# Kernel tuning notes

Hardware: AMD Instinct MI355X
Metric: run time of the kernel (lower is better)

Reference implementation:

```python
import jax, jax.numpy as jnp
import numpy as np

B, L, C, H = 2, 2048, 2048, 16
COND = 2048
HID = 4 * C
LN_EPS = 1e-6


def _ln(x):
    m = jnp.mean(x, axis=-1, keepdims=True)
    v = jnp.mean((x - m) ** 2, axis=-1, keepdims=True)
    return (x - m) / jnp.sqrt(v + LN_EPS)


def _gelu_tanh(u):
    c = np.sqrt(2.0 / np.pi).astype(np.float32)
    return 0.5 * u * (1.0 + jnp.tanh(c * (u + 0.044715 * u ** 3)))


def setup_inputs() -> dict:
    key = jax.random.key(0)
    ks = jax.random.split(key, 8)
    s = 0.02
    return {
        "x": jax.random.normal(ks[0], (B, L, C), jnp.float32),
        "cond_BD": jax.random.normal(ks[1], (B, COND), jnp.float32),
        "attn_bias": jnp.zeros((1, 1, L, L), jnp.float32),
        "Wqkv": (jax.random.normal(ks[2], (3 * C, C), jnp.float32) * s),
        "q_bias": jnp.zeros((C,), jnp.float32),
        "v_bias": jnp.zeros((C,), jnp.float32),
        "scale_mul_log": jnp.full((1, H, 1, 1), np.log(4.0), jnp.float32),
        "Wproj": (jax.random.normal(ks[3], (C, C), jnp.float32) * s),
        "bproj": jnp.zeros((C,), jnp.float32),
        "Wada": (jax.random.normal(ks[4], (6 * C, COND), jnp.float32) * s),
        "bada": jnp.zeros((6 * C,), jnp.float32),
        "Wfc1": (jax.random.normal(ks[5], (HID, C), jnp.float32) * s),
        "bfc1": jnp.zeros((HID,), jnp.float32),
        "Wfc2": (jax.random.normal(ks[6], (C, HID), jnp.float32) * s),
        "bfc2": jnp.zeros((C,), jnp.float32),
    }


def reference(x, cond_BD, attn_bias, Wqkv, q_bias, v_bias, scale_mul_log,
              Wproj, bproj, Wada, bada, Wfc1, bfc1, Wfc2, bfc2):
    Bs, Lx, Cx = x.shape
    D = Cx // H
    # AdaLN modulation: SiLU -> Linear(cond_dim, 6C) -> view(B,1,6,C).unbind(2)
    ada = (jax.nn.silu(cond_BD) @ Wada.T + bada).reshape(Bs, 1, 6, Cx)
    gamma1, gamma2, scale1, scale2, shift1, shift2 = [ada[:, :, i, :] for i in range(6)]

    def attn(xin):
        qkv_bias = jnp.concatenate([q_bias, jnp.zeros_like(q_bias), v_bias])
        qkv = (xin @ Wqkv.T + qkv_bias).reshape(Bs, Lx, 3, H, D)
        qkv = jnp.transpose(qkv, (2, 0, 3, 1, 4))  # [3, B, H, L, D]
        q, k, v = qkv[0], qkv[1], qkv[2]
        # cos-attn: L2-normalize q,k; q scaled by exp(clamped log-scale); softmax scale = 1
        sm = jnp.exp(jnp.minimum(scale_mul_log, jnp.log(jnp.float32(100.0))))
        qn = q / jnp.maximum(jnp.linalg.norm(q, axis=-1, keepdims=True), 1e-12) * sm
        kn = k / jnp.maximum(jnp.linalg.norm(k, axis=-1, keepdims=True), 1e-12)
        scores = jnp.einsum('bhqd,bhkd->bhqk', qn, kn) + attn_bias
        p = jax.nn.softmax(scores, axis=-1)
        o = jnp.einsum('bhqk,bhkd->bhqd', p, v)
        o = jnp.transpose(o, (0, 2, 1, 3)).reshape(Bs, Lx, Cx)
        return o @ Wproj.T + bproj

    x = x + attn(_ln(x) * (scale1 + 1.0) + shift1) * gamma1
    h = _gelu_tanh((_ln(x) * (scale2 + 1.0) + shift2) @ Wfc1.T + bfc1)
    x = x + (h @ Wfc2.T + bfc2) * gamma2
    return x
```

## Files before the change

### kernel.cpp

```cpp
#include <hip/hip_runtime.h>

typedef unsigned short u16;
typedef float f32x4 __attribute__((ext_vector_type(4)));
typedef short short8 __attribute__((ext_vector_type(8)));

#define C_ 2048
#define L_ 2048
#define H_ 16
#define D_ 128
#define SIXC 12288

__device__ __forceinline__ u16 f2bf(float f) {
  union { float f; unsigned u; } v; v.f = f;
  unsigned r = v.u + 0x7FFFu + ((v.u >> 16) & 1u);
  return (u16)(r >> 16);
}
__device__ __forceinline__ float bf2f(u16 b) {
  union { unsigned u; float f; } v; v.u = ((unsigned)b) << 16; return v.f;
}

#define GLOAD_LDS16(g, l)                                            \
  __builtin_amdgcn_global_load_lds(                                  \
      (__attribute__((address_space(1))) void*)(g),                  \
      (__attribute__((address_space(3))) void*)(l), 16, 0, 0)

__global__ __launch_bounds__(256) void conv_bf16(
    const float* __restrict__ src, u16* __restrict__ dst, int n) {
  int i = (blockIdx.x * 256 + threadIdx.x) * 4;
  if (i >= n) return;
  float4 v = *(const float4*)&src[i];
  ushort4 o;
  o.x = f2bf(v.x); o.y = f2bf(v.y); o.z = f2bf(v.z); o.w = f2bf(v.w);
  *(ushort4*)&dst[i] = o;
}

__global__ __launch_bounds__(256) void prep_kernel(
    const float* __restrict__ cond, const float* __restrict__ qb,
    const float* __restrict__ vb, const float* __restrict__ sml,
    float* __restrict__ silu_cond, float* __restrict__ qkvbias,
    float* __restrict__ sm) {
  int i = blockIdx.x * 256 + threadIdx.x;
  if (i < 4096) { float c = cond[i]; silu_cond[i] = c / (1.f + __expf(-c)); }
  if (i < 6144) {
    float bv = (i < 2048) ? qb[i] : ((i < 4096) ? 0.f : vb[i - 4096]);
    qkvbias[i] = bv;
  }
  if (i < 16) sm[i] = __expf(fminf(sml[i], 4.6051701859880914f));
}

__global__ __launch_bounds__(256) void ada_gemm(
    const float* __restrict__ sc, const float* __restrict__ Wada,
    const float* __restrict__ bada, float* __restrict__ ada) {
  int gw = (blockIdx.x * 256 + threadIdx.x) >> 6;
  int lane = threadIdx.x & 63;
  int b = gw / SIXC, row = gw % SIXC;
  const float* s0 = sc + b * 2048;
  const float* w0 = Wada + (size_t)row * 2048;
  float s = 0.f;
  for (int k = lane; k < 2048; k += 64) s = fmaf(s0[k], w0[k], s);
  #pragma unroll
  for (int off = 32; off; off >>= 1) s += __shfl_xor(s, off);
  if (lane == 0) ada[(size_t)b * SIXC + row] = s + bada[row];
}

__global__ __launch_bounds__(256) void ln_mod(
    const float* __restrict__ x, const float* __restrict__ ada,
    u16* __restrict__ out, int soff, int shoff) {
  int r = blockIdx.x;
  int b = r >> 11;
  int tid = threadIdx.x;
  const float* xr = x + (size_t)r * 2048;
  int c0 = tid * 8;
  float4 u0 = *(const float4*)&xr[c0];
  float4 u1 = *(const float4*)&xr[c0 + 4];
  float v[8] = {u0.x,u0.y,u0.z,u0.w,u1.x,u1.y,u1.z,u1.w};
  float s = 0.f, s2 = 0.f;
  #pragma unroll
  for (int j = 0; j < 8; ++j) { s += v[j]; s2 = fmaf(v[j], v[j], s2); }
  int wv = tid >> 6, lane = tid & 63;
  #pragma unroll
  for (int off = 32; off; off >>= 1) { s += __shfl_xor(s, off); s2 += __shfl_xor(s2, off); }
  __shared__ float red[8];
  if (!lane) { red[wv] = s; red[4 + wv] = s2; }
  __syncthreads();
  s = red[0] + red[1] + red[2] + red[3];
  s2 = red[4] + red[5] + red[6] + red[7];
  float mean = s * (1.f / 2048.f);
  float var = s2 * (1.f / 2048.f) - mean * mean;
  float rstd = rsqrtf(var + 1e-6f);
  const float* sc = ada + (size_t)b * SIXC + soff;
  const float* sh = ada + (size_t)b * SIXC + shoff;
  u16* orow = out + (size_t)r * 2048;
  #pragma unroll
  for (int j = 0; j < 8; ++j) {
    int c = c0 + j;
    float y = (v[j] - mean) * rstd * (1.f + sc[c]) + sh[c];
    orow[c] = f2bf(y);
  }
}

__global__ __launch_bounds__(256) void qk_norm_bf(
    u16* __restrict__ qb, u16* __restrict__ kb, const float* __restrict__ sm) {
  int gw = (blockIdx.x * 256 + threadIdx.x) >> 6;
  int lane = threadIdx.x & 63;
  int which = gw >> 16;
  int rid = gw & 0xFFFF;
  int h = (rid >> 11) & 15;
  u16* base = (which ? kb : qb) + (size_t)rid * 128 + lane * 2;
  unsigned uu = *(const unsigned*)base;
  float v0 = bf2f((u16)(uu & 0xFFFFu));
  float v1 = bf2f((u16)(uu >> 16));
  float ss = v0 * v0 + v1 * v1;
  #pragma unroll
  for (int off = 32; off; off >>= 1) ss += __shfl_xor(ss, off);
  float rn = 1.f / fmaxf(sqrtf(ss), 1e-12f);
  if (which == 0) rn *= sm[h];
  unsigned o = (unsigned)f2bf(v0 * rn) | ((unsigned)f2bf(v1 * rn) << 16);
  *(unsigned*)base = o;
}

#define PSP 68
__global__ __launch_bounds__(256) void attn_mfma(
    const u16* __restrict__ qb, const u16* __restrict__ kb,
    const u16* __restrict__ vbt, const float* __restrict__ bias,
    u16* __restrict__ o) {
  __shared__ u16 Ks[2][64 * 128];
  __shared__ u16 Vt[2][128 * 64];
  __shared__ u16 Ps[4][16 * PSP];
  int tid = threadIdx.x;
  int w = tid >> 6, lane = tid & 63;
  int flat = blockIdx.y * gridDim.x + blockIdx.x;
  int rl = (flat & 7) * 128 + (flat >> 3);
  int bh = rl >> 5, b = bh >> 4, h = bh & 15;
  int q0 = (rl & 31) * 64;
  int lr = lane & 15, lg = lane >> 4;
  short8 aq[4];
  {
    const u16* qrow = qb + ((size_t)bh * L_ + q0 + w * 16 + lr) * 128 + lg * 8;
    #pragma unroll
    for (int ks = 0; ks < 4; ++ks) aq[ks] = *(const short8*)(qrow + ks * 32);
  }
  f32x4 oacc[8] = {};
  float m = -1e30f, l = 0.f;
  const float* brow = bias + (size_t)(q0 + w * 16 + lr) * L_;
  const u16* kbase = kb + (size_t)bh * L_ * 128;
  const u16* vbase = vbt + (size_t)bh * 128 * L_;
  const int kq0 = tid;
  const int vq0 = tid;

  float4 brg[4], bnr[4];
  #pragma unroll
  for (int i = 0; i < 4; ++i) {
    int q = i * 256 + kq0;
    int r = q >> 4, c = q & 15;
    GLOAD_LDS16(kbase + (size_t)r * 128 + ((c ^ (r & 7)) * 8), &Ks[0][q * 8]);
  }
  #pragma unroll
  for (int i = 0; i < 4; ++i) {
    int q = i * 256 + vq0;
    int r = q >> 3, c = q & 7;
    GLOAD_LDS16(vbase + (size_t)r * L_ + ((c ^ (r & 7)) * 8), &Vt[0][q * 8]);
  }
  #pragma unroll
  for (int kg = 0; kg < 4; ++kg)
    brg[kg] = *(const float4*)&brow[kg * 16 + lg * 4];
  __syncthreads();

  for (int kt = 0; kt < 32; ++kt) {
    const int cur = kt & 1;
    if (kt < 31) {
      const int nxt = cur ^ 1;
      const u16* kb2 = kbase + (size_t)(kt + 1) * 64 * 128;
      #pragma unroll
      for (int i = 0; i < 4; ++i) {
        int q = i * 256 + kq0;
        int r = q >> 4, c = q & 15;
        GLOAD_LDS16(kb2 + (size_t)r * 128 + ((c ^ (r & 7)) * 8), &Ks[nxt][q * 8]);
      }
      #pragma unroll
      for (int i = 0; i < 4; ++i) {
        int q = i * 256 + vq0;
        int r = q >> 3, c = q & 7;
        GLOAD_LDS16(vbase + (size_t)r * L_ + (kt + 1) * 64 + ((c ^ (r & 7)) * 8),
                    &Vt[nxt][q * 8]);
      }
      #pragma unroll
      for (int kg = 0; kg < 4; ++kg)
        bnr[kg] = *(const float4*)&brow[(kt + 1) * 64 + kg * 16 + lg * 4];
    }
    f32x4 s[4] = {};
    __builtin_amdgcn_s_setprio(1);
    #pragma unroll
    for (int ks = 0; ks < 4; ++ks) {
      #pragma unroll
      for (int kg = 0; kg < 4; ++kg) {
        int row = kg * 16 + lr;
        short8 bk = *(const short8*)&Ks[cur][row * 128 + (((ks * 4 + lg) ^ (lr & 7)) * 8)];
        s[kg] = __builtin_amdgcn_mfma_f32_16x16x32_bf16(bk, aq[ks], s[kg], 0, 0, 0);
      }
    }
    __builtin_amdgcn_s_setprio(0);
    float p[4][4];
    #pragma unroll
    for (int kg = 0; kg < 4; ++kg) {
      p[kg][0] = s[kg][0] + brg[kg].x;
      p[kg][1] = s[kg][1] + brg[kg].y;
      p[kg][2] = s[kg][2] + brg[kg].z;
      p[kg][3] = s[kg][3] + brg[kg].w;
    }
    float tm = fmaxf(
        fmaxf(fmaxf(fmaxf(p[0][0], p[0][1]), fmaxf(p[0][2], p[0][3])),
              fmaxf(fmaxf(p[1][0], p[1][1]), fmaxf(p[1][2], p[1][3]))),
        fmaxf(fmaxf(fmaxf(p[2][0], p[2][1]), fmaxf(p[2][2], p[2][3])),
              fmaxf(fmaxf(p[3][0], p[3][1]), fmaxf(p[3][2], p[3][3]))));
    tm = fmaxf(tm, __shfl_xor(tm, 16));
    tm = fmaxf(tm, __shfl_xor(tm, 32));
    if (__any(tm > m + 8.f)) {
      float nm = fmaxf(m, tm);
      float a = __expf(m - nm);
      m = nm;
      l *= a;
      float al[4];
      #pragma unroll
      for (int j = 0; j < 4; ++j) al[j] = __shfl(a, lg * 4 + j);
      #pragma unroll
      for (int dg = 0; dg < 8; ++dg) {
        f32x4 t = oacc[dg];
        t[0] *= al[0]; t[1] *= al[1]; t[2] *= al[2]; t[3] *= al[3];
        oacc[dg] = t;
      }
    }
    float ps = 0.f;
    #pragma unroll
    for (int kg = 0; kg < 4; ++kg) {
      #pragma unroll
      for (int j = 0; j < 4; ++j) { p[kg][j] = __expf(p[kg][j] - m); ps += p[kg][j]; }
    }
    ps += __shfl_xor(ps, 16);
    ps += __shfl_xor(ps, 32);
    l += ps;
    #pragma unroll
    for (int kg = 0; kg < 4; ++kg) {
      unsigned lo = (unsigned)f2bf(p[kg][0]) | ((unsigned)f2bf(p[kg][1]) << 16);
      unsigned hi = (unsigned)f2bf(p[kg][2]) | ((unsigned)f2bf(p[kg][3]) << 16);
      uint2 w2; w2.x = lo; w2.y = hi;
      *(uint2*)&Ps[w][lr * PSP + kg * 16 + lg * 4] = w2;
    }
    __threadfence_block();
    short8 pa0 = *(const short8*)&Ps[w][lr * PSP + lg * 8];
    short8 pa1 = *(const short8*)&Ps[w][lr * PSP + 32 + lg * 8];
    __builtin_amdgcn_s_setprio(1);
    #pragma unroll
    for (int dg = 0; dg < 8; ++dg) {
      int row = dg * 16 + lr;
      short8 bv0 = *(const short8*)&Vt[cur][row * 64 + ((lg ^ (lr & 7)) * 8)];
      oacc[dg] = __builtin_amdgcn_mfma_f32_16x16x32_bf16(pa0, bv0, oacc[dg], 0, 0, 0);
      short8 bv1 = *(const short8*)&Vt[cur][row * 64 + (((4 + lg) ^ (lr & 7)) * 8)];
      oacc[dg] = __builtin_amdgcn_mfma_f32_16x16x32_bf16(pa1, bv1, oacc[dg], 0, 0, 0);
    }
    __builtin_amdgcn_s_setprio(0);
    __syncthreads();
    #pragma unroll
    for (int i = 0; i < 4; ++i) brg[i] = bnr[i];
  }
  float inv[4];
  #pragma unroll
  for (int j = 0; j < 4; ++j) inv[j] = 1.f / __shfl(l, lg * 4 + j);
  #pragma unroll
  for (int j = 0; j < 4; ++j) {
    u16* dst = &o[((size_t)(b * L_) + q0 + w * 16 + lg * 4 + j) * 2048 + h * 128 + lr];
    #pragma unroll
    for (int dg = 0; dg < 8; ++dg) dst[dg * 16] = f2bf(oacc[dg][j] * inv[j]);
  }
}

template <int EPI>
__global__ __launch_bounds__(256) void gemm128(
    const u16* __restrict__ A, const u16* __restrict__ W,
    const float* __restrict__ bias, const float* __restrict__ res,
    const float* __restrict__ ada, int goff,
    float* __restrict__ outf, u16* __restrict__ outb,
    u16* __restrict__ p0, u16* __restrict__ p1, u16* __restrict__ p2,
    int M, int N, int K) {
  __shared__ u16 As[2][128 * 64];
  __shared__ u16 Bs[2][128 * 64];
  const int tid = threadIdx.x;
  const int m0 = blockIdx.y * 128, n0 = blockIdx.x * 128;
  const int wv = tid >> 6, lane = tid & 63;
  const int wr = wv >> 1, wc = wv & 1;
  const int lr = lane & 15, lg = lane >> 4;
  const int sr = lane >> 3;
  const int scol = ((lane & 7) ^ sr) * 8;
  const int cswz = (lr & 7) * 8;
  f32x4 acc[4][4] = {};
  const u16* Ab = A + (size_t)m0 * K;
  const u16* Bb = W + (size_t)n0 * K;
  const int nt = K >> 6;
  #pragma unroll
  for (int p = 0; p < 4; ++p) {
    int chunk = wv * 4 + p;
    int row = chunk * 8 + sr;
    GLOAD_LDS16(Ab + (size_t)row * K + scol, &As[0][chunk * 512]);
    GLOAD_LDS16(Bb + (size_t)row * K + scol, &Bs[0][chunk * 512]);
  }
  for (int t = 0; t < nt; ++t) {
    __syncthreads();
    const int cur = t & 1;
    if (t + 1 < nt) {
      const int k0 = (t + 1) << 6;
      #pragma unroll
      for (int p = 0; p < 4; ++p) {
        int chunk = wv * 4 + p;
        int row = chunk * 8 + sr;
        GLOAD_LDS16(Ab + (size_t)row * K + k0 + scol, &As[cur ^ 1][chunk * 512]);
        GLOAD_LDS16(Bb + (size_t)row * K + k0 + scol, &Bs[cur ^ 1][chunk * 512]);
      }
    }
    #pragma unroll
    for (int kk = 0; kk < 2; ++kk) {
      short8 af[4], bfr[4];
      const int col = (kk * 32 + lg * 8) ^ cswz;
      #pragma unroll
      for (int i = 0; i < 4; ++i) {
        af[i]  = *(const short8*)&As[cur][(wr * 64 + i * 16 + lr) * 64 + col];
        bfr[i] = *(const short8*)&Bs[cur][(wc * 64 + i * 16 + lr) * 64 + col];
      }
      #pragma unroll
      for (int mi = 0; mi < 4; ++mi)
        #pragma unroll
        for (int ni = 0; ni < 4; ++ni)
          acc[mi][ni] = __builtin_amdgcn_mfma_f32_16x16x32_bf16(af[mi], bfr[ni], acc[mi][ni], 0, 0, 0);
    }
  }
  #pragma unroll
  for (int mi = 0; mi < 4; ++mi) {
    #pragma unroll
    for (int ni = 0; ni < 4; ++ni) {
      int gcol = n0 + wc * 64 + ni * 16 + lr;
      float bv = bias[gcol];
      #pragma unroll
      for (int j = 0; j < 4; ++j) {
        int grow = m0 + wr * 64 + mi * 16 + lg * 4 + j;
        float v = acc[mi][ni][j] + bv;
        if (EPI == 0) {
          int which = gcol >> 11;
          int h = (gcol >> 7) & 15;
          int d = gcol & 127;
          int b = grow >> 11, ll = grow & 2047;
          int bh = b * 16 + h;
          if (which == 0)      p0[((size_t)bh * L_ + ll) * 128 + d] = f2bf(v);
          else if (which == 1) p1[((size_t)bh * L_ + ll) * 128 + d] = f2bf(v);
          else                 p2[((size_t)bh * 128 + d) * L_ + ll] = f2bf(v);
        } else if (EPI == 1) {
          float u = 0.7978845608028654f * (v + 0.044715f * v * v * v);
          float e = __expf(2.f * u);
          float th = 1.f - 2.f / (e + 1.f);
          outb[(size_t)grow * N + gcol] = f2bf(0.5f * v * (1.f + th));
        } else {
          int b = grow >> 11;
          float g = ada[(size_t)b * SIXC + goff + gcol];
          size_t oi = (size_t)grow * N + gcol;
          outf[oi] = res[oi] + v * g;
        }
      }
    }
  }
}

extern "C" void kernel_launch(void* const* d_in, const int* in_sizes, int n_in,
                              void* d_out, int out_size, void* d_ws, size_t ws_size,
                              hipStream_t stream) {
  const float* x        = (const float*)d_in[0];
  const float* cond     = (const float*)d_in[1];
  const float* attnbias = (const float*)d_in[2];
  const float* Wqkv     = (const float*)d_in[3];
  const float* q_bias   = (const float*)d_in[4];
  const float* v_bias   = (const float*)d_in[5];
  const float* sml      = (const float*)d_in[6];
  const float* Wproj    = (const float*)d_in[7];
  const float* bproj    = (const float*)d_in[8];
  const float* Wada     = (const float*)d_in[9];
  const float* bada     = (const float*)d_in[10];
  const float* Wfc1     = (const float*)d_in[11];
  const float* bfc1     = (const float*)d_in[12];
  const float* Wfc2     = (const float*)d_in[13];
  const float* bfc2     = (const float*)d_in[14];
  float* out = (float*)d_out;
  char* ws = (char*)d_ws;
  const size_t MB = 1ull << 20;

  float* silu_cond = (float*)(ws + 0);
  float* qkvbias   = (float*)(ws + (16 << 10));
  float* smbuf     = (float*)(ws + (40 << 10));
  float* adab      = (float*)(ws + (48 << 10));
  u16*   xob       = (u16*)(ws + 1 * MB);
  u16*   qbb       = (u16*)(ws + 17 * MB);
  u16*   kbb       = (u16*)(ws + 33 * MB);
  float* x1        = (float*)(ws + 17 * MB);
  u16*   vbt       = (u16*)(ws + 49 * MB);
  u16*   hbuf      = (u16*)(ws + 49 * MB);
  u16*   wqkv_bf   = (u16*)(ws + 65 * MB);
  u16*   wproj_bf  = (u16*)(ws + 89 * MB);
  u16*   wfc1_bf   = (u16*)(ws + 113 * MB);
  u16*   wfc2_bf   = (u16*)(ws + 145 * MB);

  conv_bf16<<<12288, 256, 0, stream>>>(Wqkv, wqkv_bf, 6144 * 2048);
  conv_bf16<<<4096, 256, 0, stream>>>(Wproj, wproj_bf, 2048 * 2048);
  conv_bf16<<<16384, 256, 0, stream>>>(Wfc1, wfc1_bf, 8192 * 2048);
  conv_bf16<<<16384, 256, 0, stream>>>(Wfc2, wfc2_bf, 2048 * 8192);
  prep_kernel<<<24, 256, 0, stream>>>(cond, q_bias, v_bias, sml, silu_cond, qkvbias, smbuf);
  ada_gemm<<<6144, 256, 0, stream>>>(silu_cond, Wada, bada, adab);
  ln_mod<<<4096, 256, 0, stream>>>(x, adab, xob, 2 * C_, 4 * C_);
  gemm128<0><<<dim3(48, 32), 256, 0, stream>>>(xob, wqkv_bf, qkvbias, nullptr, nullptr, 0,
                                               nullptr, nullptr, qbb, kbb, vbt, 4096, 6144, 2048);
  qk_norm_bf<<<32768, 256, 0, stream>>>(qbb, kbb, smbuf);
  attn_mfma<<<dim3(32, 32), 256, 0, stream>>>(qbb, kbb, vbt, attnbias, xob);
  gemm128<2><<<dim3(16, 32), 256, 0, stream>>>(xob, wproj_bf, bproj, x, adab, 0,
                                               x1, nullptr, nullptr, nullptr, nullptr, 4096, 2048, 2048);
  ln_mod<<<4096, 256, 0, stream>>>(x1, adab, xob, 3 * C_, 5 * C_);
  gemm128<1><<<dim3(64, 32), 256, 0, stream>>>(xob, wfc1_bf, bfc1, nullptr, nullptr, 0,
                                               nullptr, hbuf, nullptr, nullptr, nullptr, 4096, 8192, 2048);
  gemm128<2><<<dim3(16, 32), 256, 0, stream>>>(hbuf, wfc2_bf, bfc2, x1, adab, C_,
                                               out, nullptr, nullptr, nullptr, nullptr, 4096, 2048, 8192);
}
```

Baseline: 818.3 us.

## Replace 128x128 GEMM with 8-wave 256-wide tile kernel using explicit vmcnt pipelining

Replaces the 4-wave 128x128 GEMM with an 8-wave kernel that uses 256-column tiles (256 or 128 rows), explicit vmcnt waits and raw barriers, so the next tile's global-to-LDS loads overlap the MFMA work. The MFMA phases are split into halves with setprio and sched barriers. Larger tiles increase operand reuse and cut global traffic per FLOP, at the cost of more LDS and registers and fewer blocks. The ada_gemm loop is also vectorised to float4 loads.

```diff
diff --git a/kernel.cpp b/kernel.cpp
--- a/kernel.cpp
+++ b/kernel.cpp
@@ -23,6 +23,12 @@
   __builtin_amdgcn_global_load_lds(                                  \
       (__attribute__((address_space(1))) void*)(g),                  \
       (__attribute__((address_space(3))) void*)(l), 16, 0, 0)
+
+template <int N> __device__ __forceinline__ void wait_vmcnt() {
+  if constexpr (N == 8)      asm volatile("s_waitcnt vmcnt(8)" ::: "memory");
+  else if constexpr (N == 6) asm volatile("s_waitcnt vmcnt(6)" ::: "memory");
+  else                       asm volatile("s_waitcnt vmcnt(0)" ::: "memory");
+}
 
 __global__ __launch_bounds__(256) void conv_bf16(
     const float* __restrict__ src, u16* __restrict__ dst, int n) {
@@ -57,7 +63,12 @@
   const float* s0 = sc + b * 2048;
   const float* w0 = Wada + (size_t)row * 2048;
   float s = 0.f;
-  for (int k = lane; k < 2048; k += 64) s = fmaf(s0[k], w0[k], s);
+  for (int k = lane * 4; k < 2048; k += 256) {
+    float4 a = *(const float4*)&s0[k];
+    float4 w = *(const float4*)&w0[k];
+    s = fmaf(a.x, w.x, s); s = fmaf(a.y, w.y, s);
+    s = fmaf(a.z, w.z, s); s = fmaf(a.w, w.w, s);
+  }
   #pragma unroll
   for (int off = 32; off; off >>= 1) s += __shfl_xor(s, off);
   if (lane == 0) ada[(size_t)b * SIXC + row] = s + bada[row];
@@ -274,75 +285,123 @@
   }
 }
 
-template <int EPI>
-__global__ __launch_bounds__(256) void gemm128(
+template <int BM, int EPI>
+__global__ __launch_bounds__(512, 2) void gemm8p(
     const u16* __restrict__ A, const u16* __restrict__ W,
     const float* __restrict__ bias, const float* __restrict__ res,
     const float* __restrict__ ada, int goff,
     float* __restrict__ outf, u16* __restrict__ outb,
     u16* __restrict__ p0, u16* __restrict__ p1, u16* __restrict__ p2,
     int M, int N, int K) {
-  __shared__ u16 As[2][128 * 64];
-  __shared__ u16 Bs[2][128 * 64];
+  constexpr int MI  = BM / 32;
+  constexpr int MIH = MI / 2;
+  constexpr int LA  = BM / 64;
+  constexpr int VMW = LA + 4;
+  __shared__ __attribute__((aligned(16))) u16 As[2][BM * 64];
+  __shared__ __attribute__((aligned(16))) u16 Bs[2][256 * 64];
   const int tid = threadIdx.x;
-  const int m0 = blockIdx.y * 128, n0 = blockIdx.x * 128;
+  const int m0 = blockIdx.y * BM, n0 = blockIdx.x * 256;
   const int wv = tid >> 6, lane = tid & 63;
-  const int wr = wv >> 1, wc = wv & 1;
+  const int wr = wv >> 2, wc = wv & 3;
   const int lr = lane & 15, lg = lane >> 4;
   const int sr = lane >> 3;
   const int scol = ((lane & 7) ^ sr) * 8;
   const int cswz = (lr & 7) * 8;
-  f32x4 acc[4][4] = {};
+  f32x4 acc[MI][4] = {};
   const u16* Ab = A + (size_t)m0 * K;
   const u16* Bb = W + (size_t)n0 * K;
   const int nt = K >> 6;
-  #pragma unroll
-  for (int p = 0; p < 4; ++p) {
-    int chunk = wv * 4 + p;
-    int row = chunk * 8 + sr;
-    GLOAD_LDS16(Ab + (size_t)row * K + scol, &As[0][chunk * 512]);
-    GLOAD_LDS16(Bb + (size_t)row * K + scol, &Bs[0][chunk * 512]);
-  }
+
+  auto stage = [&](int bi, int k0) {
+    #pragma unroll
+    for (int p = 0; p < LA; ++p) {
+      int chunk = wv * LA + p;
+      int row = chunk * 8 + sr;
+      GLOAD_LDS16(Ab + (size_t)row * K + k0 + scol, &As[bi][chunk * 512]);
+    }
+    #pragma unroll
+    for (int p = 0; p < 4; ++p) {
+      int chunk = wv * 4 + p;
+      int row = chunk * 8 + sr;
+      GLOAD_LDS16(Bb + (size_t)row * K + k0 + scol, &Bs[bi][chunk * 512]);
+    }
+  };
+
+  stage(0, 0);
   for (int t = 0; t < nt; ++t) {
-    __syncthreads();
     const int cur = t & 1;
     if (t + 1 < nt) {
-      const int k0 = (t + 1) << 6;
-      #pragma unroll
-      for (int p = 0; p < 4; ++p) {
-        int chunk = wv * 4 + p;
-        int row = chunk * 8 + sr;
-        GLOAD_LDS16(Ab + (size_t)row * K + k0 + scol, &As[cur ^ 1][chunk * 512]);
-        GLOAD_LDS16(Bb + (size_t)row * K + k0 + scol, &Bs[cur ^ 1][chunk * 512]);
-      }
-    }
-    #pragma unroll
-    for (int kk = 0; kk < 2; ++kk) {
-      short8 af[4], bfr[4];
-      const int col = (kk * 32 + lg * 8) ^ cswz;
-      #pragma unroll
-      for (int i = 0; i < 4; ++i) {
-        af[i]  = *(const short8*)&As[cur][(wr * 64 + i * 16 + lr) * 64 + col];
-        bfr[i] = *(const short8*)&Bs[cur][(wc * 64 + i * 16 + lr) * 64 + col];
-      }
-      #pragma unroll
-      for (int mi = 0; mi < 4; ++mi)
+      stage(cur ^ 1, (t + 1) << 6);
+      wait_vmcnt<VMW>();
+    } else {
+      wait_vmcnt<0>();
+    }
+    __builtin_amdgcn_s_barrier();
+    __builtin_amdgcn_sched_barrier(0);
+    short8 bf[4][2];
+    #pragma unroll
+    for (int mh = 0; mh < 2; ++mh) {
+      short8 af[MIH][2];
+      #pragma unroll
+      for (int kk = 0; kk < 2; ++kk) {
+        const int col = (kk * 32 + lg * 8) ^ cswz;
         #pragma unroll
-        for (int ni = 0; ni < 4; ++ni)
-          acc[mi][ni] = __builtin_amdgcn_mfma_f32_16x16x32_bf16(af[mi], bfr[ni], acc[mi][ni], 0, 0, 0);
-    }
-  }
-  #pragma unroll
-  for (int mi = 0; mi < 4; ++mi) {
+        for (int i = 0; i < MIH; ++i)
+          af[i][kk] = *(const short8*)
+              &As[cur][(wr * (BM / 2) + (mh * MIH + i) * 16 + lr) * 64 + col];
+        if (mh == 0) {
+          #pragma unroll
+          for (int i = 0; i < 4; ++i)
+            bf[i][kk] = *(const short8*)
+                &Bs[cur][(wc * 64 + i * 16 + lr) * 64 + col];
+        }
+      }
+      asm volatile("s_waitcnt lgkmcnt(0)" ::: "memory");
+      __builtin_amdgcn_sched_barrier(0);
+      if constexpr (BM == 256) {
+        #pragma unroll
+        for (int nh = 0; nh < 2; ++nh) {
+          __builtin_amdgcn_s_setprio(1);
+          #pragma unroll
+          for (int kk = 0; kk < 2; ++kk)
+            #pragma unroll
+            for (int i = 0; i < MIH; ++i)
+              #pragma unroll
+              for (int jn = 0; jn < 2; ++jn)
+                acc[mh * MIH + i][nh * 2 + jn] =
+                    __builtin_amdgcn_mfma_f32_16x16x32_bf16(
+                        af[i][kk], bf[nh * 2 + jn][kk],
+                        acc[mh * MIH + i][nh * 2 + jn], 0, 0, 0);
+          __builtin_amdgcn_s_setprio(0);
+          __builtin_amdgcn_s_barrier();
+        }
+      } else {
+        __builtin_amdgcn_s_setprio(1);
+        #pragma unroll
+        for (int kk = 0; kk < 2; ++kk)
+          #pragma unroll
+          for (int i = 0; i < MIH; ++i)
+            #pragma unroll
+            for (int jn = 0; jn < 4; ++jn)
+              acc[mh * MIH + i][jn] = __builtin_amdgcn_mfma_f32_16x16x32_bf16(
+                  af[i][kk], bf[jn][kk], acc[mh * MIH + i][jn], 0, 0, 0);
+        __builtin_amdgcn_s_setprio(0);
+        __builtin_amdgcn_s_barrier();
+      }
+    }
+    __builtin_amdgcn_sched_barrier(0);
+  }
+  #pragma unroll
+  for (int mi = 0; mi < MI; ++mi) {
     #pragma unroll
     for (int ni = 0; ni < 4; ++ni) {
       int gcol = n0 + wc * 64 + ni * 16 + lr;
       float bv = bias[gcol];
       #pragma unroll
       for (int j = 0; j < 4; ++j) {
-        int grow = m0 + wr * 64 + mi * 16 + lg * 4 + j;
+        int grow = m0 + wr * (BM / 2) + mi * 16 + lg * 4 + j;
         float v = acc[mi][ni][j] + bv;
-        if (EPI == 0) {
+        if constexpr (EPI == 0) {
           int which = gcol >> 11;
           int h = (gcol >> 7) & 15;
           int d = gcol & 127;
@@ -351,7 +410,7 @@
           if (which == 0)      p0[((size_t)bh * L_ + ll) * 128 + d] = f2bf(v);
           else if (which == 1) p1[((size_t)bh * L_ + ll) * 128 + d] = f2bf(v);
           else                 p2[((size_t)bh * 128 + d) * L_ + ll] = f2bf(v);
-        } else if (EPI == 1) {
+        } else if constexpr (EPI == 1) {
           float u = 0.7978845608028654f * (v + 0.044715f * v * v * v);
           float e = __expf(2.f * u);
           float th = 1.f - 2.f / (e + 1.f);
@@ -411,15 +470,15 @@
   prep_kernel<<<24, 256, 0, stream>>>(cond, q_bias, v_bias, sml, silu_cond, qkvbias, smbuf);
   ada_gemm<<<6144, 256, 0, stream>>>(silu_cond, Wada, bada, adab);
   ln_mod<<<4096, 256, 0, stream>>>(x, adab, xob, 2 * C_, 4 * C_);
-  gemm128<0><<<dim3(48, 32), 256, 0, stream>>>(xob, wqkv_bf, qkvbias, nullptr, nullptr, 0,
-                                               nullptr, nullptr, qbb, kbb, vbt, 4096, 6144, 2048);
+  gemm8p<256, 0><<<dim3(24, 16), 512, 0, stream>>>(xob, wqkv_bf, qkvbias, nullptr, nullptr, 0,
+      nullptr, nullptr, qbb, kbb, vbt, 4096, 6144, 2048);
   qk_norm_bf<<<32768, 256, 0, stream>>>(qbb, kbb, smbuf);
   attn_mfma<<<dim3(32, 32), 256, 0, stream>>>(qbb, kbb, vbt, attnbias, xob);
-  gemm128<2><<<dim3(16, 32), 256, 0, stream>>>(xob, wproj_bf, bproj, x, adab, 0,
-                                               x1, nullptr, nullptr, nullptr, nullptr, 4096, 2048, 2048);
+  gemm8p<128, 2><<<dim3(8, 32), 512, 0, stream>>>(xob, wproj_bf, bproj, x, adab, 0,
+      x1, nullptr, nullptr, nullptr, nullptr, 4096, 2048, 2048);
   ln_mod<<<4096, 256, 0, stream>>>(x1, adab, xob, 3 * C_, 5 * C_);
-  gemm128<1><<<dim3(64, 32), 256, 0, stream>>>(xob, wfc1_bf, bfc1, nullptr, nullptr, 0,
-                                               nullptr, hbuf, nullptr, nullptr, nullptr, 4096, 8192, 2048);
-  gemm128<2><<<dim3(16, 32), 256, 0, stream>>>(hbuf, wfc2_bf, bfc2, x1, adab, C_,
-                                               out, nullptr, nullptr, nullptr, nullptr, 4096, 2048, 8192);
-}
+  gemm8p<256, 1><<<dim3(32, 16), 512, 0, stream>>>(xob, wfc1_bf, bfc1, nullptr, nullptr, 0,
+      nullptr, hbuf, nullptr, nullptr, nullptr, 4096, 8192, 2048);
+  gemm8p<128, 2><<<dim3(8, 32), 512, 0, stream>>>(hbuf, wfc2_bf, bfc2, x1, adab, C_,
+      out, nullptr, nullptr, nullptr, nullptr, 4096, 2048, 8192);
+}
```

Measured after the change: 908.2 us. 11.0% more time.

## Prefetch two GEMM tiles ahead with manual vmcnt waits and swizzled tile order

Applied to the files above, without the earlier changes.

Reworks the main bf16 GEMM loop so each block issues loads for the stage two k-steps ahead. Before each compute step it waits only until the current stage's global-to-LDS loads have landed (vmcnt), and it uses explicit barriers in place of __syncthreads. Block indices are also remapped with an 8-way interleave to change the order in which output tiles are scheduled, aiming for better L2 reuse. The AdaLN matvec is vectorized to float4 loads. The hand-written waitcnt and barrier sequence relies on exact counting of outstanding loads and is fragile if the instruction scheduling changes.

```diff
diff --git a/kernel.cpp b/kernel.cpp
--- a/kernel.cpp
+++ b/kernel.cpp
@@ -23,6 +23,12 @@
   __builtin_amdgcn_global_load_lds(                                  \
       (__attribute__((address_space(1))) void*)(g),                  \
       (__attribute__((address_space(3))) void*)(l), 16, 0, 0)
+
+template <int N> __device__ __forceinline__ void wait_vmcnt() {
+  if constexpr (N == 8)      asm volatile("s_waitcnt vmcnt(8)" ::: "memory");
+  else if constexpr (N == 6) asm volatile("s_waitcnt vmcnt(6)" ::: "memory");
+  else                       asm volatile("s_waitcnt vmcnt(0)" ::: "memory");
+}
 
 __global__ __launch_bounds__(256) void conv_bf16(
     const float* __restrict__ src, u16* __restrict__ dst, int n) {
@@ -57,7 +63,12 @@
   const float* s0 = sc + b * 2048;
   const float* w0 = Wada + (size_t)row * 2048;
   float s = 0.f;
-  for (int k = lane; k < 2048; k += 64) s = fmaf(s0[k], w0[k], s);
+  for (int k = lane * 4; k < 2048; k += 256) {
+    float4 a = *(const float4*)&s0[k];
+    float4 w = *(const float4*)&w0[k];
+    s = fmaf(a.x, w.x, s); s = fmaf(a.y, w.y, s);
+    s = fmaf(a.z, w.z, s); s = fmaf(a.w, w.w, s);
+  }
   #pragma unroll
   for (int off = 32; off; off >>= 1) s += __shfl_xor(s, off);
   if (lane == 0) ada[(size_t)b * SIXC + row] = s + bada[row];
@@ -285,7 +296,10 @@
   __shared__ u16 As[2][128 * 64];
   __shared__ u16 Bs[2][128 * 64];
   const int tid = threadIdx.x;
-  const int m0 = blockIdx.y * 128, n0 = blockIdx.x * 128;
+  const int nwg = gridDim.x * gridDim.y;
+  const int flat = blockIdx.y * gridDim.x + blockIdx.x;
+  const int swz = (flat & 7) * (nwg >> 3) + (flat >> 3);
+  const int m0 = (swz / gridDim.x) * 128, n0 = (swz % gridDim.x) * 128;
   const int wv = tid >> 6, lane = tid & 63;
   const int wr = wv >> 1, wc = wv & 1;
   const int lr = lane & 15, lg = lane >> 4;
@@ -296,26 +310,22 @@
   const u16* Ab = A + (size_t)m0 * K;
   const u16* Bb = W + (size_t)n0 * K;
   const int nt = K >> 6;
-  #pragma unroll
-  for (int p = 0; p < 4; ++p) {
-    int chunk = wv * 4 + p;
-    int row = chunk * 8 + sr;
-    GLOAD_LDS16(Ab + (size_t)row * K + scol, &As[0][chunk * 512]);
-    GLOAD_LDS16(Bb + (size_t)row * K + scol, &Bs[0][chunk * 512]);
-  }
+  auto stage = [&](int bi, int k0) {
+    #pragma unroll
+    for (int p = 0; p < 4; ++p) {
+      int chunk = wv * 4 + p;
+      int row = chunk * 8 + sr;
+      GLOAD_LDS16(Ab + (size_t)row * K + k0 + scol, &As[bi][chunk * 512]);
+      GLOAD_LDS16(Bb + (size_t)row * K + k0 + scol, &Bs[bi][chunk * 512]);
+    }
+  };
+  stage(0, 0);
+  stage(1, 64);
   for (int t = 0; t < nt; ++t) {
-    __syncthreads();
     const int cur = t & 1;
-    if (t + 1 < nt) {
-      const int k0 = (t + 1) << 6;
-      #pragma unroll
-      for (int p = 0; p < 4; ++p) {
-        int chunk = wv * 4 + p;
-        int row = chunk * 8 + sr;
-        GLOAD_LDS16(Ab + (size_t)row * K + k0 + scol, &As[cur ^ 1][chunk * 512]);
-        GLOAD_LDS16(Bb + (size_t)row * K + k0 + scol, &Bs[cur ^ 1][chunk * 512]);
-      }
-    }
+    if (t + 1 < nt) wait_vmcnt<8>(); else wait_vmcnt<0>();
+    __builtin_amdgcn_s_barrier();
+    __builtin_amdgcn_sched_barrier(0);
     #pragma unroll
     for (int kk = 0; kk < 2; ++kk) {
       short8 af[4], bfr[4];
@@ -331,6 +341,11 @@
         for (int ni = 0; ni < 4; ++ni)
           acc[mi][ni] = __builtin_amdgcn_mfma_f32_16x16x32_bf16(af[mi], bfr[ni], acc[mi][ni], 0, 0, 0);
     }
+    __builtin_amdgcn_sched_barrier(0);
+    asm volatile("s_waitcnt lgkmcnt(0)" ::: "memory");
+    __builtin_amdgcn_s_barrier();
+    __builtin_amdgcn_sched_barrier(0);
+    if (t + 2 < nt) stage(cur, (t + 2) << 6);
   }
   #pragma unroll
   for (int mi = 0; mi < 4; ++mi) {
```

After: 812.4 us. Within noise of the previous version (-0.7%).
